# Optimization experiments

Measured on AMD Instinct MI355X. Metric: run time of the kernel, lower is better.

The kernel has to match this reference:

```python
import jax, jax.numpy as jnp
import numpy as np

DIM = 256
NUM_HEADS = 4
HEAD_DIM = DIM // NUM_HEADS
MLP_HIDDEN = int(DIM * 2.0)
SCALE = HEAD_DIM ** -0.5
LN_EPS = 1e-5


def _layernorm(x, gamma, beta):
    mu = jnp.mean(x, axis=-1, keepdims=True)
    var = jnp.mean(jnp.square(x - mu), axis=-1, keepdims=True)
    return (x - mu) * jax.lax.rsqrt(var + LN_EPS) * gamma + beta


def setup_inputs() -> dict:
    key = jax.random.key(0)
    ks = jax.random.split(key, 8)
    B, C, N, P = 8, DIM, 64, 256
    s = 0.02
    return {
        "x": jax.random.normal(ks[0], (B, C, N, P), dtype=jnp.float32),
        # torch Linear weights stored [out_features, in_features]
        "W_qkv": jax.random.normal(ks[1], (3 * DIM, DIM), dtype=jnp.float32) * s,
        "W_proj": jax.random.normal(ks[2], (DIM, DIM), dtype=jnp.float32) * s,
        "b_proj": jnp.zeros((DIM,), dtype=jnp.float32),
        "ln1_g": jnp.ones((DIM,), dtype=jnp.float32),
        "ln1_b": jnp.zeros((DIM,), dtype=jnp.float32),
        "ln2_g": jnp.ones((DIM,), dtype=jnp.float32),
        "ln2_b": jnp.zeros((DIM,), dtype=jnp.float32),
        "W_mlp1": jax.random.normal(ks[3], (MLP_HIDDEN, DIM), dtype=jnp.float32) * s,
        "b_mlp1": jnp.zeros((MLP_HIDDEN,), dtype=jnp.float32),
        "W_mlp2": jax.random.normal(ks[4], (DIM, MLP_HIDDEN), dtype=jnp.float32) * s,
        "b_mlp2": jnp.zeros((DIM,), dtype=jnp.float32),
    }


def reference(x, W_qkv, W_proj, b_proj, ln1_g, ln1_b, ln2_g, ln2_b,
              W_mlp1, b_mlp1, W_mlp2, b_mlp2):
    B, C, N, P = x.shape
    H, D = NUM_HEADS, HEAD_DIM
    # [B,C,N,P] -> [B*N, P, C]
    x_seq = jnp.transpose(x, (0, 2, 3, 1)).reshape(B * N, P, C)
    shortcut = x_seq

    h = _layernorm(x_seq, ln1_g, ln1_b)
    qkv = jnp.einsum('spc,oc->spo', h, W_qkv)              # [BN, P, 3C]
    qkv = qkv.reshape(B * N, P, 3, H, D)
    q = jnp.transpose(qkv[:, :, 0], (0, 2, 1, 3))          # [BN, H, P, D]
    k = jnp.transpose(qkv[:, :, 1], (0, 2, 1, 3))
    v = jnp.transpose(qkv[:, :, 2], (0, 2, 1, 3))

    attn = jnp.einsum('shpd,shqd->shpq', q, k) * SCALE     # [BN, H, P, P]
    attn = jax.nn.softmax(attn, axis=-1)
    o = jnp.einsum('shpq,shqd->shpd', attn, v)             # [BN, H, P, D]
    o = jnp.transpose(o, (0, 2, 1, 3)).reshape(B * N, P, C)
    o = jnp.einsum('spc,oc->spo', o, W_proj) + b_proj

    x_seq = shortcut + o

    h2 = _layernorm(x_seq, ln2_g, ln2_b)
    m = jnp.einsum('spc,oc->spo', h2, W_mlp1) + b_mlp1
    m = jax.nn.gelu(m, approximate=False)
    m = jnp.einsum('sph,oh->spo', m, W_mlp2) + b_mlp2
    x_seq = x_seq + m

    out = x_seq.reshape(B, N, P, C)
    return jnp.transpose(out, (0, 3, 1, 2))                # [B, C, N, P]
```

## Files before the change

### kernel.cpp

```cpp
#include <hip/hip_runtime.h>
#include <stdint.h>
#include <math.h>


#define DEV static __device__ __forceinline__

typedef __bf16 bf16x8 __attribute__((ext_vector_type(8)));
typedef float  f32x4  __attribute__((ext_vector_type(4)));

union B8 { bf16x8 v; uint4 q; uint32_t u[4]; uint16_t h[8]; };

DEV uint16_t f2bf(float f) {
  uint32_t u = __float_as_uint(f);
  return (uint16_t)((u + 0x7FFFu + ((u >> 16) & 1u)) >> 16);
}
DEV float bf2f(uint16_t h) { return __uint_as_float(((uint32_t)h) << 16); }
DEV uint32_t pk2(float a, float b) { return (uint32_t)f2bf(a) | ((uint32_t)f2bf(b) << 16); }

DEV f32x4 mfma16(const B8& a, const B8& b, f32x4 c) {
  return __builtin_amdgcn_mfma_f32_16x16x32_bf16(a.v, b.v, c, 0, 0, 0);
}

DEV uint32_t shfl_u(uint32_t v, int src) { return (uint32_t)__shfl((int)v, src, 64); }

DEV B8 mk(const uint32_t* w) {
  B8 x; x.u[0] = w[0]; x.u[1] = w[1]; x.u[2] = w[2]; x.u[3] = w[3]; return x;
}

DEV void xpose(const uint32_t* pk0, const uint32_t* pk1, int kd, int g, int r, uint32_t* out) {
  const int sA = 32 * (g & 1) + r;
  const int sB = sA + 16;
  const int tA = 2 * kd, tB = 2 * kd + 1;
  uint32_t a0 = shfl_u(pk0[tA], sA), b0 = shfl_u(pk0[tB], sA);
  uint32_t a1 = shfl_u(pk1[tA], sA), b1 = shfl_u(pk1[tB], sA);
  uint32_t a2 = shfl_u(pk0[tA], sB), b2 = shfl_u(pk0[tB], sB);
  uint32_t a3 = shfl_u(pk1[tA], sB), b3 = shfl_u(pk1[tB], sB);
  const bool hi = g >= 2;
  out[0] = hi ? b0 : a0;
  out[1] = hi ? b1 : a1;
  out[2] = hi ? b2 : a2;
  out[3] = hi ? b3 : a3;
}

__global__ void transformer_prep(const float* __restrict__ wqkv,
                                 const float* __restrict__ wproj,
                                 const float* __restrict__ w1,
                                 const float* __restrict__ w2,
                                 uint16_t* __restrict__ dst) {
  int e = blockIdx.x * 256 + threadIdx.x;
  const float* src; int C, local;
  if (e < 196608)      { src = wqkv;  C = 256; local = e; }
  else if (e < 262144) { src = wproj; C = 256; local = e - 196608; }
  else if (e < 393216) { src = w1;    C = 256; local = e - 262144; }
  else                 { src = w2;    C = 512; local = e - 393216; }
  int k32 = C >> 5;
  int tile = local >> 9, within = local & 511;
  int ln = within >> 3, j = within & 7;
  int tr = tile / k32, tk = tile - tr * k32;
  int row = tr * 16 + (ln & 15), col = tk * 32 + (ln >> 4) * 8 + j;
  float v = src[row * C + col];
  if (e < 65536) v *= 0.18033688011112042f;
  dst[e] = f2bf(v);
}

__global__ __launch_bounds__(1024, 4) void transformer_k1(
    const float* __restrict__ x,
    const float* __restrict__ bproj,
    const float* __restrict__ ln1g, const float* __restrict__ ln1b,
    const uint16_t* __restrict__ wf,
    uint16_t* __restrict__ osc,
    float* __restrict__ out) {
  __shared__ __attribute__((aligned(16))) uint8_t lds[65536];
  const int tid = threadIdx.x;
  const int lane = tid & 63;
  const int w = tid >> 6;
  const int r = lane & 15;
  const int g = lane >> 4;
  const int s = blockIdx.x;
  const int bb = s >> 6, nn = s & 63;
  const float* xs = x + (size_t)bb * 4194304 + (size_t)nn * 256;
  float* outp = out + (size_t)bb * 4194304 + (size_t)nn * 256;
  const f32x4 fz = {0.f, 0.f, 0.f, 0.f};

  uint32_t hfrag[8][4];
  {
    float s1 = 0.f, s2 = 0.f;
    const int p = 16 * w + r;
#pragma unroll
    for (int kt = 0; kt < 8; ++kt) {
      int c0 = 32 * kt + 8 * g;
      float v[8];
#pragma unroll
      for (int j = 0; j < 8; ++j) {
        v[j] = xs[(size_t)(c0 + j) * 16384 + p];
        s1 += v[j];
        s2 += v[j] * v[j];
      }
#pragma unroll
      for (int q = 0; q < 4; ++q) hfrag[kt][q] = pk2(v[2 * q], v[2 * q + 1]);
    }
    s1 += __shfl_xor(s1, 16, 64); s1 += __shfl_xor(s1, 32, 64);
    s2 += __shfl_xor(s2, 16, 64); s2 += __shfl_xor(s2, 32, 64);
    float mu = s1 * (1.0f / 256.0f);
    float var = s2 * (1.0f / 256.0f) - mu * mu;
    float rs = rsqrtf(var + 1e-5f);
#pragma unroll
    for (int kt = 0; kt < 8; ++kt) {
      int c0 = 32 * kt + 8 * g;
      f32x4 gA = *(const f32x4*)(ln1g + c0), gB = *(const f32x4*)(ln1g + c0 + 4);
      f32x4 bA = *(const f32x4*)(ln1b + c0), bB = *(const f32x4*)(ln1b + c0 + 4);
#pragma unroll
      for (int q = 0; q < 4; ++q) {
        uint32_t pw = hfrag[kt][q];
        float lo = bf2f((uint16_t)(pw & 0xFFFFu));
        float hi = bf2f((uint16_t)(pw >> 16));
        float glo = (q < 2) ? gA[2 * q] : gB[2 * q - 4];
        float ghi = (q < 2) ? gA[2 * q + 1] : gB[2 * q - 3];
        float blo = (q < 2) ? bA[2 * q] : bB[2 * q - 4];
        float bhi = (q < 2) ? bA[2 * q + 1] : bB[2 * q - 3];
        lo = (lo - mu) * rs * glo + blo;
        hi = (hi - mu) * rs * ghi + bhi;
        hfrag[kt][q] = pk2(lo, hi);
      }
    }
  }

#pragma unroll 1
  for (int hd = 0; hd < 4; ++hd) {
#pragma unroll
    for (int m = 0; m < 2; ++m) {
      f32x4 acc[4];
#pragma unroll
      for (int ct = 0; ct < 4; ++ct) acc[ct] = fz;
#pragma unroll
      for (int kt = 0; kt < 8; ++kt) {
        B8 a = mk(hfrag[kt]);
#pragma unroll
        for (int ct = 0; ct < 4; ++ct) {
          B8 wfr;
          wfr.q = *(const uint4*)(wf + (size_t)((((m + 1) * 16 + hd * 4 + ct) * 8 + kt) * 512) + lane * 8);
          acc[ct] = mfma16(a, wfr, acc[ct]);
        }
      }
#pragma unroll
      for (int ct = 0; ct < 4; ++ct) {
        int d = 16 * ct + r;
        int q0 = 16 * w + 4 * g;
        if (m == 0) {
#pragma unroll
          for (int i = 0; i < 4; ++i) {
            int qq = q0 + i;
            *(uint16_t*)(lds + ((qq * 128 + d * 2) ^ ((qq & 7) << 4))) = f2bf(acc[ct][i]);
          }
        } else {
          uint2 pv;
          pv.x = pk2(acc[ct][0], acc[ct][1]);
          pv.y = pk2(acc[ct][2], acc[ct][3]);
          *(uint2*)(lds + ((32768 + d * 512 + q0 * 2) ^ ((d & 7) << 4))) = pv;
        }
      }
    }
    __syncthreads();

    {
      f32x4 qT[4];
#pragma unroll
      for (int mt = 0; mt < 4; ++mt) qT[mt] = fz;
#pragma unroll
      for (int kt = 0; kt < 8; ++kt) {
        B8 hb = mk(hfrag[kt]);
#pragma unroll
        for (int mt = 0; mt < 4; ++mt) {
          B8 wa;
          wa.q = *(const uint4*)(wf + (size_t)(((hd * 4 + mt) * 8 + kt) * 512) + lane * 8);
          qT[mt] = mfma16(wa, hb, qT[mt]);
        }
      }
      uint32_t pq0[4], pq1[4];
#pragma unroll
      for (int mt = 0; mt < 4; ++mt) {
        pq0[mt] = pk2(qT[mt][0], qT[mt][1]);
        pq1[mt] = pk2(qT[mt][2], qT[mt][3]);
      }
      uint32_t qb[2][4];
#pragma unroll
      for (int kd = 0; kd < 2; ++kd) xpose(pq0, pq1, kd, g, r, qb[kd]);

      float m_ = -1e30f, l_ = 0.f;
      f32x4 oT[4];
#pragma unroll
      for (int dt = 0; dt < 4; ++dt) oT[dt] = fz;

#pragma unroll 1
      for (int chk = 0; chk < 4; ++chk) {
        f32x4 sT[4];
#pragma unroll
        for (int qt = 0; qt < 4; ++qt) sT[qt] = fz;
#pragma unroll
        for (int kd = 0; kd < 2; ++kd) {
          B8 qf = mk(qb[kd]);
#pragma unroll
          for (int qt = 0; qt < 4; ++qt) {
            int qq = chk * 64 + 16 * qt + r;
            B8 ka;
            ka.q = *(const uint4*)(lds + ((qq * 128 + (32 * kd + 8 * g) * 2) ^ ((qq & 7) << 4)));
            sT[qt] = mfma16(ka, qf, sT[qt]);
          }
        }
        float tmax = sT[0][0];
#pragma unroll
        for (int qt = 0; qt < 4; ++qt)
#pragma unroll
          for (int i = 0; i < 4; ++i) tmax = fmaxf(tmax, sT[qt][i]);
        tmax = fmaxf(tmax, __shfl_xor(tmax, 16, 64));
        tmax = fmaxf(tmax, __shfl_xor(tmax, 32, 64));
        float mn = fmaxf(m_, tmax);
        float fcor = exp2f(m_ - mn);
        float ts = 0.f;
#pragma unroll
        for (int qt = 0; qt < 4; ++qt)
#pragma unroll
          for (int i = 0; i < 4; ++i) {
            float e = exp2f(sT[qt][i] - mn);
            sT[qt][i] = e;
            ts += e;
          }
        ts += __shfl_xor(ts, 16, 64);
        ts += __shfl_xor(ts, 32, 64);
        l_ = l_ * fcor + ts;
        m_ = mn;
#pragma unroll
        for (int dt = 0; dt < 4; ++dt)
#pragma unroll
          for (int i = 0; i < 4; ++i) oT[dt][i] *= fcor;
        uint32_t pp0[4], pp1[4];
#pragma unroll
        for (int qt = 0; qt < 4; ++qt) {
          pp0[qt] = pk2(sT[qt][0], sT[qt][1]);
          pp1[qt] = pk2(sT[qt][2], sT[qt][3]);
        }
#pragma unroll
        for (int qk = 0; qk < 2; ++qk) {
          uint32_t pb[4];
          xpose(pp0, pp1, qk, g, r, pb);
          B8 pf = mk(pb);
#pragma unroll
          for (int dt = 0; dt < 4; ++dt) {
            B8 va;
            va.q = *(const uint4*)(lds + ((32768 + (16 * dt + r) * 512 + (chk * 64 + 32 * qk + 8 * g) * 2) ^ ((r & 7) << 4)));
            oT[dt] = mfma16(va, pf, oT[dt]);
          }
        }
      }
      float inv = 1.0f / l_;
      uint32_t po0[4], po1[4];
#pragma unroll
      for (int dt = 0; dt < 4; ++dt) {
        po0[dt] = pk2(oT[dt][0] * inv, oT[dt][1] * inv);
        po1[dt] = pk2(oT[dt][2] * inv, oT[dt][3] * inv);
      }
#pragma unroll
      for (int kd = 0; kd < 2; ++kd) {
        uint32_t ofr[4];
        xpose(po0, po1, kd, g, r, ofr);
        B8 t; t.u[0] = ofr[0]; t.u[1] = ofr[1]; t.u[2] = ofr[2]; t.u[3] = ofr[3];
        *(uint4*)(osc + (size_t)((s * 16 + w) * 8 + 2 * hd + kd) * 512 + lane * 8) = t.q;
      }
    }
    __syncthreads();
  }

#pragma unroll 1
  for (int q3 = 0; q3 < 4; ++q3) {
    f32x4 acc[4];
#pragma unroll
    for (int ct = 0; ct < 4; ++ct) acc[ct] = fz;
#pragma unroll
    for (int kt = 0; kt < 8; ++kt) {
      B8 a;
      a.q = *(const uint4*)(osc + (size_t)((s * 16 + w) * 8 + kt) * 512 + lane * 8);
#pragma unroll
      for (int ct = 0; ct < 4; ++ct) {
        B8 wfr;
        wfr.q = *(const uint4*)(wf + 196608 + (size_t)(((q3 * 4 + ct) * 8 + kt) * 512) + lane * 8);
        acc[ct] = mfma16(a, wfr, acc[ct]);
      }
    }
#pragma unroll
    for (int ct = 0; ct < 4; ++ct) {
      int c = q3 * 64 + 16 * ct + r;
      float bias = bproj[c];
      int p0 = 16 * w + 4 * g;
      f32x4 res = *(const f32x4*)(xs + (size_t)c * 16384 + p0);
      f32x4 x2v;
#pragma unroll
      for (int i = 0; i < 4; ++i) x2v[i] = acc[ct][i] + bias + res[i];
      *(f32x4*)(outp + (size_t)c * 16384 + p0) = x2v;
    }
  }
}

__global__ __launch_bounds__(1024, 4) void transformer_k2(
    const float* __restrict__ ln2g, const float* __restrict__ ln2b,
    const uint16_t* __restrict__ w1f, const uint16_t* __restrict__ w2f,
    const float* __restrict__ bm1, const float* __restrict__ bm2,
    float* __restrict__ out) {
  __shared__ __attribute__((aligned(16))) uint8_t lds[106496];
  const int tid = threadIdx.x;
  const int lane = tid & 63;
  const int w = tid >> 6;
  const int r = lane & 15, g = lane >> 4;
  const int bid = blockIdx.x;
  const int s = bid >> 2, tg = bid & 3;
  const int bb = s >> 6, nn = s & 63;
  float* outp = out + (size_t)bb * 4194304 + (size_t)nn * 256;
  const int tokbase = tg * 64;
  const f32x4 fz = {0.f, 0.f, 0.f, 0.f};

  float v[16];
  {
    float s1 = 0.f, s2 = 0.f;
    const int p = tokbase + lane;
#pragma unroll
    for (int j = 0; j < 16; ++j) {
      float t = outp[(size_t)(w * 16 + j) * 16384 + p];
      v[j] = t;
      s1 += t;
      s2 += t * t;
    }
    float2 pr; pr.x = s1; pr.y = s2;
    *(float2*)(lds + 98304 + (w * 64 + lane) * 8) = pr;
  }
  __syncthreads();
  {
    float su = 0.f, sq = 0.f;
#pragma unroll
    for (int w2 = 0; w2 < 16; ++w2) {
      float2 pr = *(const float2*)(lds + 98304 + (w2 * 64 + lane) * 8);
      su += pr.x;
      sq += pr.y;
    }
    float mu = su * (1.0f / 256.0f);
    float var = sq * (1.0f / 256.0f) - mu * mu;
    float rs = rsqrtf(var + 1e-5f);
    uint32_t pk[8];
#pragma unroll
    for (int q = 0; q < 4; ++q) {
      int c0 = w * 16 + q * 4;
      f32x4 gv = *(const f32x4*)(ln2g + c0);
      f32x4 bv = *(const f32x4*)(ln2b + c0);
      float n0 = (v[q * 4 + 0] - mu) * rs * gv[0] + bv[0];
      float n1 = (v[q * 4 + 1] - mu) * rs * gv[1] + bv[1];
      float n2 = (v[q * 4 + 2] - mu) * rs * gv[2] + bv[2];
      float n3 = (v[q * 4 + 3] - mu) * rs * gv[3] + bv[3];
      pk[q * 2 + 0] = pk2(n0, n1);
      pk[q * 2 + 1] = pk2(n2, n3);
    }
    const int mt = lane >> 4;
    const int kt = w >> 1;
#pragma unroll
    for (int hblk = 0; hblk < 2; ++hblk) {
      int lanep = (lane & 15) + 32 * (w & 1) + 16 * hblk;
      uint4 t;
      t.x = pk[hblk * 4 + 0]; t.y = pk[hblk * 4 + 1];
      t.z = pk[hblk * 4 + 2]; t.w = pk[hblk * 4 + 3];
      *(uint4*)(lds + (mt * 8 + kt) * 1024 + lanep * 16) = t;
    }
  }
  __syncthreads();

  f32x4 acc1[4][2];
#pragma unroll
  for (int mt = 0; mt < 4; ++mt)
#pragma unroll
    for (int nt = 0; nt < 2; ++nt) acc1[mt][nt] = fz;
#pragma unroll
  for (int kt = 0; kt < 8; ++kt) {
    B8 a[4];
#pragma unroll
    for (int mt = 0; mt < 4; ++mt)
      a[mt].q = *(const uint4*)(lds + (mt * 8 + kt) * 1024 + lane * 16);
#pragma unroll
    for (int nt = 0; nt < 2; ++nt) {
      B8 bfr;
      bfr.q = *(const uint4*)(w1f + (size_t)(((2 * w + nt) * 8 + kt) * 512) + lane * 8);
#pragma unroll
      for (int mt = 0; mt < 4; ++mt) acc1[mt][nt] = mfma16(a[mt], bfr, acc1[mt][nt]);
    }
  }
#pragma unroll
  for (int nt = 0; nt < 2; ++nt) {
    float bias = bm1[(2 * w + nt) * 16 + r];
#pragma unroll
    for (int mt = 0; mt < 4; ++mt) {
#pragma unroll
      for (int i = 0; i < 4; ++i) {
        float vv = acc1[mt][nt][i] + bias;
        vv = 0.5f * vv * (1.0f + erff(vv * 0.70710678118654752440f));
        int lanep = (4 * g + i) + 16 * (2 * nt + (r >> 3));
        *(uint16_t*)(lds + 32768 + (mt * 16 + w) * 1024 + lanep * 16 + (r & 7) * 2) = f2bf(vv);
      }
    }
  }
  __syncthreads();

  f32x4 acc2[4];
#pragma unroll
  for (int mt = 0; mt < 4; ++mt) acc2[mt] = fz;
#pragma unroll
  for (int kt = 0; kt < 16; ++kt) {
    B8 bfr;
    bfr.q = *(const uint4*)(w2f + (size_t)((w * 16 + kt) * 512) + lane * 8);
#pragma unroll
    for (int mt = 0; mt < 4; ++mt) {
      B8 a;
      a.q = *(const uint4*)(lds + 32768 + (mt * 16 + kt) * 1024 + lane * 16);
      acc2[mt] = mfma16(a, bfr, acc2[mt]);
    }
  }

  {
    int c = w * 16 + r;
    float bias = bm2[c];
#pragma unroll
    for (int mt = 0; mt < 4; ++mt) {
      int p0 = tokbase + 16 * mt + 4 * g;
      f32x4 res = *(const f32x4*)(outp + (size_t)c * 16384 + p0);
      f32x4 o;
#pragma unroll
      for (int i = 0; i < 4; ++i) o[i] = res[i] + acc2[mt][i] + bias;
      *(f32x4*)(outp + (size_t)c * 16384 + p0) = o;
    }
  }
}

extern "C" void kernel_launch(void* const* d_in, const int* in_sizes, int n_in,
                              void* d_out, int out_size, void* d_ws, size_t ws_size,
                              hipStream_t stream) {
  (void)in_sizes; (void)n_in; (void)out_size; (void)ws_size;
  const float* x     = (const float*)d_in[0];
  const float* wqkv  = (const float*)d_in[1];
  const float* wproj = (const float*)d_in[2];
  const float* bproj = (const float*)d_in[3];
  const float* ln1g  = (const float*)d_in[4];
  const float* ln1b  = (const float*)d_in[5];
  const float* ln2g  = (const float*)d_in[6];
  const float* ln2b  = (const float*)d_in[7];
  const float* w1    = (const float*)d_in[8];
  const float* bm1   = (const float*)d_in[9];
  const float* w2    = (const float*)d_in[10];
  const float* bm2   = (const float*)d_in[11];
  uint16_t* wbf = (uint16_t*)d_ws;
  uint16_t* osc = wbf + 524288;
  float* out = (float*)d_out;

  transformer_prep<<<2048, 256, 0, stream>>>(wqkv, wproj, w1, w2, wbf);
  transformer_k1<<<512, 1024, 0, stream>>>(x, bproj, ln1g, ln1b, wbf, osc, out);
  transformer_k2<<<2048, 1024, 0, stream>>>(ln2g, ln2b, wbf + 262144, wbf + 393216, bm1, bm2, out);
}
```

Baseline: 710.5 us.

## Split fused transformer block into five staged kernels with global intermediates

Replaces the two large fused kernels (attention block per sequence with 1024 threads, MLP block) with five 256-thread kernels: LN1+QKV projection writing Q/K/V fragments to workspace, per-head attention, output projection plus residual with LN2 statistics, MLP1 with GELU, and MLP2 plus residual. The intent is finer-grained parallelism, higher occupancy and larger per-wave MFMA tiles, in place of one block serially looping over heads. The cost is large bf16 intermediate traffic through global memory (Q, K, V, MLP hidden activations) and extra kernel launches.

```diff
diff --git a/kernel.cpp b/kernel.cpp
--- a/kernel.cpp
+++ b/kernel.cpp
@@ -20,11 +20,18 @@
 DEV f32x4 mfma16(const B8& a, const B8& b, f32x4 c) {
   return __builtin_amdgcn_mfma_f32_16x16x32_bf16(a.v, b.v, c, 0, 0, 0);
 }
-
 DEV uint32_t shfl_u(uint32_t v, int src) { return (uint32_t)__shfl((int)v, src, 64); }
-
-DEV B8 mk(const uint32_t* w) {
-  B8 x; x.u[0] = w[0]; x.u[1] = w[1]; x.u[2] = w[2]; x.u[3] = w[3]; return x;
+DEV f32x4 vmax4(f32x4 a, f32x4 b) {
+  f32x4 o;
+  o[0] = fmaxf(a[0], b[0]); o[1] = fmaxf(a[1], b[1]);
+  o[2] = fmaxf(a[2], b[2]); o[3] = fmaxf(a[3], b[3]);
+  return o;
+}
+DEV f32x4 shfl4x(f32x4 v, int m) {
+  f32x4 o;
+#pragma unroll
+  for (int i = 0; i < 4; ++i) o[i] = __shfl_xor(v[i], m, 64);
+  return o;
 }
 
 DEV void xpose(const uint32_t* pk0, const uint32_t* pk1, int kd, int g, int r, uint32_t* out) {
@@ -63,373 +70,517 @@
   dst[e] = f2bf(v);
 }
 
-__global__ __launch_bounds__(1024, 4) void transformer_k1(
+__global__ __launch_bounds__(256, 2) void transformer_kA(
     const float* __restrict__ x,
-    const float* __restrict__ bproj,
     const float* __restrict__ ln1g, const float* __restrict__ ln1b,
-    const uint16_t* __restrict__ wf,
-    uint16_t* __restrict__ osc,
-    float* __restrict__ out) {
-  __shared__ __attribute__((aligned(16))) uint8_t lds[65536];
+    const uint16_t* __restrict__ wqkvf,
+    uint16_t* __restrict__ qf, uint16_t* __restrict__ kf,
+    uint16_t* __restrict__ vt) {
+  __shared__ __attribute__((aligned(16))) uint8_t lds[76800];
   const int tid = threadIdx.x;
   const int lane = tid & 63;
-  const int w = tid >> 6;
-  const int r = lane & 15;
-  const int g = lane >> 4;
-  const int s = blockIdx.x;
-  const int bb = s >> 6, nn = s & 63;
-  const float* xs = x + (size_t)bb * 4194304 + (size_t)nn * 256;
-  float* outp = out + (size_t)bb * 4194304 + (size_t)nn * 256;
-  const f32x4 fz = {0.f, 0.f, 0.f, 0.f};
-
-  uint32_t hfrag[8][4];
-  {
-    float s1 = 0.f, s2 = 0.f;
-    const int p = 16 * w + r;
-#pragma unroll
-    for (int kt = 0; kt < 8; ++kt) {
-      int c0 = 32 * kt + 8 * g;
-      float v[8];
-#pragma unroll
-      for (int j = 0; j < 8; ++j) {
-        v[j] = xs[(size_t)(c0 + j) * 16384 + p];
-        s1 += v[j];
-        s2 += v[j] * v[j];
-      }
-#pragma unroll
-      for (int q = 0; q < 4; ++q) hfrag[kt][q] = pk2(v[2 * q], v[2 * q + 1]);
-    }
-    s1 += __shfl_xor(s1, 16, 64); s1 += __shfl_xor(s1, 32, 64);
-    s2 += __shfl_xor(s2, 16, 64); s2 += __shfl_xor(s2, 32, 64);
-    float mu = s1 * (1.0f / 256.0f);
-    float var = s2 * (1.0f / 256.0f) - mu * mu;
-    float rs = rsqrtf(var + 1e-5f);
-#pragma unroll
-    for (int kt = 0; kt < 8; ++kt) {
-      int c0 = 32 * kt + 8 * g;
-      f32x4 gA = *(const f32x4*)(ln1g + c0), gB = *(const f32x4*)(ln1g + c0 + 4);
-      f32x4 bA = *(const f32x4*)(ln1b + c0), bB = *(const f32x4*)(ln1b + c0 + 4);
-#pragma unroll
-      for (int q = 0; q < 4; ++q) {
-        uint32_t pw = hfrag[kt][q];
-        float lo = bf2f((uint16_t)(pw & 0xFFFFu));
-        float hi = bf2f((uint16_t)(pw >> 16));
-        float glo = (q < 2) ? gA[2 * q] : gB[2 * q - 4];
-        float ghi = (q < 2) ? gA[2 * q + 1] : gB[2 * q - 3];
-        float blo = (q < 2) ? bA[2 * q] : bB[2 * q - 4];
-        float bhi = (q < 2) ? bA[2 * q + 1] : bB[2 * q - 3];
-        lo = (lo - mu) * rs * glo + blo;
-        hi = (hi - mu) * rs * ghi + bhi;
-        hfrag[kt][q] = pk2(lo, hi);
-      }
-    }
-  }
-
-#pragma unroll 1
-  for (int hd = 0; hd < 4; ++hd) {
-#pragma unroll
-    for (int m = 0; m < 2; ++m) {
-      f32x4 acc[4];
-#pragma unroll
-      for (int ct = 0; ct < 4; ++ct) acc[ct] = fz;
-#pragma unroll
-      for (int kt = 0; kt < 8; ++kt) {
-        B8 a = mk(hfrag[kt]);
-#pragma unroll
-        for (int ct = 0; ct < 4; ++ct) {
-          B8 wfr;
-          wfr.q = *(const uint4*)(wf + (size_t)((((m + 1) * 16 + hd * 4 + ct) * 8 + kt) * 512) + lane * 8);
-          acc[ct] = mfma16(a, wfr, acc[ct]);
-        }
-      }
-#pragma unroll
-      for (int ct = 0; ct < 4; ++ct) {
-        int d = 16 * ct + r;
-        int q0 = 16 * w + 4 * g;
-        if (m == 0) {
-#pragma unroll
-          for (int i = 0; i < 4; ++i) {
-            int qq = q0 + i;
-            *(uint16_t*)(lds + ((qq * 128 + d * 2) ^ ((qq & 7) << 4))) = f2bf(acc[ct][i]);
-          }
-        } else {
-          uint2 pv;
-          pv.x = pk2(acc[ct][0], acc[ct][1]);
-          pv.y = pk2(acc[ct][2], acc[ct][3]);
-          *(uint2*)(lds + ((32768 + d * 512 + q0 * 2) ^ ((d & 7) << 4))) = pv;
-        }
-      }
-    }
-    __syncthreads();
-
-    {
-      f32x4 qT[4];
-#pragma unroll
-      for (int mt = 0; mt < 4; ++mt) qT[mt] = fz;
-#pragma unroll
-      for (int kt = 0; kt < 8; ++kt) {
-        B8 hb = mk(hfrag[kt]);
-#pragma unroll
-        for (int mt = 0; mt < 4; ++mt) {
-          B8 wa;
-          wa.q = *(const uint4*)(wf + (size_t)(((hd * 4 + mt) * 8 + kt) * 512) + lane * 8);
-          qT[mt] = mfma16(wa, hb, qT[mt]);
-        }
-      }
-      uint32_t pq0[4], pq1[4];
-#pragma unroll
-      for (int mt = 0; mt < 4; ++mt) {
-        pq0[mt] = pk2(qT[mt][0], qT[mt][1]);
-        pq1[mt] = pk2(qT[mt][2], qT[mt][3]);
-      }
-      uint32_t qb[2][4];
-#pragma unroll
-      for (int kd = 0; kd < 2; ++kd) xpose(pq0, pq1, kd, g, r, qb[kd]);
-
-      float m_ = -1e30f, l_ = 0.f;
-      f32x4 oT[4];
-#pragma unroll
-      for (int dt = 0; dt < 4; ++dt) oT[dt] = fz;
-
-#pragma unroll 1
-      for (int chk = 0; chk < 4; ++chk) {
-        f32x4 sT[4];
-#pragma unroll
-        for (int qt = 0; qt < 4; ++qt) sT[qt] = fz;
-#pragma unroll
-        for (int kd = 0; kd < 2; ++kd) {
-          B8 qf = mk(qb[kd]);
-#pragma unroll
-          for (int qt = 0; qt < 4; ++qt) {
-            int qq = chk * 64 + 16 * qt + r;
-            B8 ka;
-            ka.q = *(const uint4*)(lds + ((qq * 128 + (32 * kd + 8 * g) * 2) ^ ((qq & 7) << 4)));
-            sT[qt] = mfma16(ka, qf, sT[qt]);
-          }
-        }
-        float tmax = sT[0][0];
-#pragma unroll
-        for (int qt = 0; qt < 4; ++qt)
-#pragma unroll
-          for (int i = 0; i < 4; ++i) tmax = fmaxf(tmax, sT[qt][i]);
-        tmax = fmaxf(tmax, __shfl_xor(tmax, 16, 64));
-        tmax = fmaxf(tmax, __shfl_xor(tmax, 32, 64));
-        float mn = fmaxf(m_, tmax);
-        float fcor = exp2f(m_ - mn);
-        float ts = 0.f;
-#pragma unroll
-        for (int qt = 0; qt < 4; ++qt)
-#pragma unroll
-          for (int i = 0; i < 4; ++i) {
-            float e = exp2f(sT[qt][i] - mn);
-            sT[qt][i] = e;
-            ts += e;
-          }
-        ts += __shfl_xor(ts, 16, 64);
-        ts += __shfl_xor(ts, 32, 64);
-        l_ = l_ * fcor + ts;
-        m_ = mn;
-#pragma unroll
-        for (int dt = 0; dt < 4; ++dt)
-#pragma unroll
-          for (int i = 0; i < 4; ++i) oT[dt][i] *= fcor;
-        uint32_t pp0[4], pp1[4];
-#pragma unroll
-        for (int qt = 0; qt < 4; ++qt) {
-          pp0[qt] = pk2(sT[qt][0], sT[qt][1]);
-          pp1[qt] = pk2(sT[qt][2], sT[qt][3]);
-        }
-#pragma unroll
-        for (int qk = 0; qk < 2; ++qk) {
-          uint32_t pb[4];
-          xpose(pp0, pp1, qk, g, r, pb);
-          B8 pf = mk(pb);
-#pragma unroll
-          for (int dt = 0; dt < 4; ++dt) {
-            B8 va;
-            va.q = *(const uint4*)(lds + ((32768 + (16 * dt + r) * 512 + (chk * 64 + 32 * qk + 8 * g) * 2) ^ ((r & 7) << 4)));
-            oT[dt] = mfma16(va, pf, oT[dt]);
-          }
-        }
-      }
-      float inv = 1.0f / l_;
-      uint32_t po0[4], po1[4];
-#pragma unroll
-      for (int dt = 0; dt < 4; ++dt) {
-        po0[dt] = pk2(oT[dt][0] * inv, oT[dt][1] * inv);
-        po1[dt] = pk2(oT[dt][2] * inv, oT[dt][3] * inv);
-      }
-#pragma unroll
-      for (int kd = 0; kd < 2; ++kd) {
-        uint32_t ofr[4];
-        xpose(po0, po1, kd, g, r, ofr);
-        B8 t; t.u[0] = ofr[0]; t.u[1] = ofr[1]; t.u[2] = ofr[2]; t.u[3] = ofr[3];
-        *(uint4*)(osc + (size_t)((s * 16 + w) * 8 + 2 * hd + kd) * 512 + lane * 8) = t.q;
-      }
-    }
-    __syncthreads();
-  }
-
-#pragma unroll 1
-  for (int q3 = 0; q3 < 4; ++q3) {
-    f32x4 acc[4];
-#pragma unroll
-    for (int ct = 0; ct < 4; ++ct) acc[ct] = fz;
-#pragma unroll
-    for (int kt = 0; kt < 8; ++kt) {
-      B8 a;
-      a.q = *(const uint4*)(osc + (size_t)((s * 16 + w) * 8 + kt) * 512 + lane * 8);
-#pragma unroll
-      for (int ct = 0; ct < 4; ++ct) {
-        B8 wfr;
-        wfr.q = *(const uint4*)(wf + 196608 + (size_t)(((q3 * 4 + ct) * 8 + kt) * 512) + lane * 8);
-        acc[ct] = mfma16(a, wfr, acc[ct]);
-      }
-    }
-#pragma unroll
-    for (int ct = 0; ct < 4; ++ct) {
-      int c = q3 * 64 + 16 * ct + r;
-      float bias = bproj[c];
-      int p0 = 16 * w + 4 * g;
-      f32x4 res = *(const f32x4*)(xs + (size_t)c * 16384 + p0);
-      f32x4 x2v;
-#pragma unroll
-      for (int i = 0; i < 4; ++i) x2v[i] = acc[ct][i] + bias + res[i];
-      *(f32x4*)(outp + (size_t)c * 16384 + p0) = x2v;
-    }
-  }
-}
-
-__global__ __launch_bounds__(1024, 4) void transformer_k2(
-    const float* __restrict__ ln2g, const float* __restrict__ ln2b,
-    const uint16_t* __restrict__ w1f, const uint16_t* __restrict__ w2f,
-    const float* __restrict__ bm1, const float* __restrict__ bm2,
-    float* __restrict__ out) {
-  __shared__ __attribute__((aligned(16))) uint8_t lds[106496];
-  const int tid = threadIdx.x;
-  const int lane = tid & 63;
-  const int w = tid >> 6;
+  const int wv = tid >> 6;
   const int r = lane & 15, g = lane >> 4;
   const int bid = blockIdx.x;
-  const int s = bid >> 2, tg = bid & 3;
-  const int bb = s >> 6, nn = s & 63;
-  float* outp = out + (size_t)bb * 4194304 + (size_t)nn * 256;
-  const int tokbase = tg * 64;
+  const int s = bid >> 2, q64 = bid & 3;
+  const int tok0 = q64 * 64;
+  const float* xs = x + (size_t)(s >> 6) * 4194304 + (size_t)(s & 63) * 256 + tok0;
   const f32x4 fz = {0.f, 0.f, 0.f, 0.f};
 
-  float v[16];
+  ((float*)(lds + 74752))[tid] = ln1g[tid];
+  ((float*)(lds + 75776))[tid] = ln1b[tid];
+
   {
-    float s1 = 0.f, s2 = 0.f;
-    const int p = tokbase + lane;
+    const int pg = tid & 15, cq = tid >> 4;
+    const int p4 = pg * 4;
+    f32x4 s1 = fz, s2 = fz;
 #pragma unroll
     for (int j = 0; j < 16; ++j) {
-      float t = outp[(size_t)(w * 16 + j) * 16384 + p];
-      v[j] = t;
-      s1 += t;
-      s2 += t * t;
-    }
-    float2 pr; pr.x = s1; pr.y = s2;
-    *(float2*)(lds + 98304 + (w * 64 + lane) * 8) = pr;
+      int c = j * 16 + cq;
+      f32x4 v = *(const f32x4*)(xs + (size_t)c * 16384 + p4);
+      s1 += v; s2 += v * v;
+      uint2 w; w.x = pk2(v[0], v[1]); w.y = pk2(v[2], v[3]);
+      *(uint2*)(lds + c * 132 + p4 * 2) = w;
+    }
+    *(f32x4*)(lds + 66560 + (cq * 16 + pg) * 32) = s1;
+    *(f32x4*)(lds + 66560 + (cq * 16 + pg) * 32 + 16) = s2;
   }
   __syncthreads();
+
   {
+    const int tokl = 16 * wv + r;
+    const int pg = tokl >> 2, e = tokl & 3;
     float su = 0.f, sq = 0.f;
 #pragma unroll
-    for (int w2 = 0; w2 < 16; ++w2) {
-      float2 pr = *(const float2*)(lds + 98304 + (w2 * 64 + lane) * 8);
-      su += pr.x;
-      sq += pr.y;
+    for (int cq = 0; cq < 16; ++cq) {
+      su += *(const float*)(lds + 66560 + (cq * 16 + pg) * 32 + e * 4);
+      sq += *(const float*)(lds + 66560 + (cq * 16 + pg) * 32 + 16 + e * 4);
     }
     float mu = su * (1.0f / 256.0f);
     float var = sq * (1.0f / 256.0f) - mu * mu;
     float rs = rsqrtf(var + 1e-5f);
-    uint32_t pk[8];
-#pragma unroll
-    for (int q = 0; q < 4; ++q) {
-      int c0 = w * 16 + q * 4;
-      f32x4 gv = *(const f32x4*)(ln2g + c0);
-      f32x4 bv = *(const f32x4*)(ln2b + c0);
-      float n0 = (v[q * 4 + 0] - mu) * rs * gv[0] + bv[0];
-      float n1 = (v[q * 4 + 1] - mu) * rs * gv[1] + bv[1];
-      float n2 = (v[q * 4 + 2] - mu) * rs * gv[2] + bv[2];
-      float n3 = (v[q * 4 + 3] - mu) * rs * gv[3] + bv[3];
-      pk[q * 2 + 0] = pk2(n0, n1);
-      pk[q * 2 + 1] = pk2(n2, n3);
-    }
-    const int mt = lane >> 4;
-    const int kt = w >> 1;
-#pragma unroll
-    for (int hblk = 0; hblk < 2; ++hblk) {
-      int lanep = (lane & 15) + 32 * (w & 1) + 16 * hblk;
-      uint4 t;
-      t.x = pk[hblk * 4 + 0]; t.y = pk[hblk * 4 + 1];
-      t.z = pk[hblk * 4 + 2]; t.w = pk[hblk * 4 + 3];
-      *(uint4*)(lds + (mt * 8 + kt) * 1024 + lanep * 16) = t;
+#pragma unroll
+    for (int tk = 0; tk < 8; ++tk) {
+      int c0 = 32 * tk + 8 * g;
+      uint32_t pk[4];
+#pragma unroll
+      for (int q = 0; q < 4; ++q) {
+        float lo, hi;
+        {
+          int c = c0 + 2 * q;
+          uint16_t raw = *(const uint16_t*)(lds + c * 132 + tokl * 2);
+          float gg = ((const float*)(lds + 74752))[c];
+          float bb = ((const float*)(lds + 75776))[c];
+          lo = (bf2f(raw) - mu) * rs * gg + bb;
+        }
+        {
+          int c = c0 + 2 * q + 1;
+          uint16_t raw = *(const uint16_t*)(lds + c * 132 + tokl * 2);
+          float gg = ((const float*)(lds + 74752))[c];
+          float bb = ((const float*)(lds + 75776))[c];
+          hi = (bf2f(raw) - mu) * rs * gg + bb;
+        }
+        pk[q] = pk2(lo, hi);
+      }
+      uint4 t; t.x = pk[0]; t.y = pk[1]; t.z = pk[2]; t.w = pk[3];
+      *(uint4*)(lds + 33792 + (wv * 8 + tk) * 1024 + lane * 16) = t;
     }
   }
   __syncthreads();
 
-  f32x4 acc1[4][2];
-#pragma unroll
-  for (int mt = 0; mt < 4; ++mt)
-#pragma unroll
-    for (int nt = 0; nt < 2; ++nt) acc1[mt][nt] = fz;
+#pragma unroll 1
+  for (int pp = 0; pp < 3; ++pp) {
+    const int n0 = wv * 192 + pp * 64;
+    const int mi = n0 >> 8, hd = (n0 >> 6) & 3;
+    const int s4hd = s * 4 + hd;
+    f32x4 acc[4][4];
+#pragma unroll
+    for (int a = 0; a < 4; ++a)
+#pragma unroll
+      for (int b = 0; b < 4; ++b) acc[a][b] = fz;
+
+    if (mi < 2) {
+#pragma unroll
+      for (int kt = 0; kt < 8; ++kt) {
+        B8 hf[4];
+#pragma unroll
+        for (int tt = 0; tt < 4; ++tt)
+          hf[tt].q = *(const uint4*)(lds + 33792 + (tt * 8 + kt) * 1024 + lane * 16);
+#pragma unroll
+        for (int nt = 0; nt < 4; ++nt) {
+          B8 wf_;
+          wf_.q = *(const uint4*)(wqkvf + (size_t)((((n0 >> 4) + nt) * 8 + kt) * 512) + lane * 8);
+#pragma unroll
+          for (int tt = 0; tt < 4; ++tt) acc[nt][tt] = mfma16(wf_, hf[tt], acc[nt][tt]);
+        }
+      }
+      uint16_t* dstb = (mi == 0) ? qf : kf;
+#pragma unroll
+      for (int tt = 0; tt < 4; ++tt) {
+        uint32_t p0[4], p1[4];
+#pragma unroll
+        for (int nt = 0; nt < 4; ++nt) {
+          p0[nt] = pk2(acc[nt][tt][0], acc[nt][tt][1]);
+          p1[nt] = pk2(acc[nt][tt][2], acc[nt][tt][3]);
+        }
+        int qtg = q64 * 4 + tt;
+#pragma unroll
+        for (int kd = 0; kd < 2; ++kd) {
+          uint32_t ofr[4];
+          xpose(p0, p1, kd, g, r, ofr);
+          uint4 t; t.x = ofr[0]; t.y = ofr[1]; t.z = ofr[2]; t.w = ofr[3];
+          *(uint4*)(dstb + (size_t)(((s4hd * 16 + qtg) * 2 + kd) * 512) + lane * 8) = t;
+        }
+      }
+    } else {
+#pragma unroll
+      for (int kt = 0; kt < 8; ++kt) {
+        B8 hf[4];
+#pragma unroll
+        for (int rt = 0; rt < 4; ++rt)
+          hf[rt].q = *(const uint4*)(lds + 33792 + (rt * 8 + kt) * 1024 + lane * 16);
+#pragma unroll
+        for (int ct = 0; ct < 4; ++ct) {
+          B8 wf_;
+          wf_.q = *(const uint4*)(wqkvf + (size_t)((((n0 >> 4) + ct) * 8 + kt) * 512) + lane * 8);
+#pragma unroll
+          for (int rt = 0; rt < 4; ++rt) acc[rt][ct] = mfma16(hf[rt], wf_, acc[rt][ct]);
+        }
+      }
+#pragma unroll
+      for (int rt = 0; rt < 4; ++rt) {
+#pragma unroll
+        for (int ct = 0; ct < 4; ++ct) {
+          int d = 16 * ct + r;
+          int tokr = tok0 + 16 * rt + 4 * g;
+          uint2 pv;
+          pv.x = pk2(acc[rt][ct][0], acc[rt][ct][1]);
+          pv.y = pk2(acc[rt][ct][2], acc[rt][ct][3]);
+          *(uint2*)(vt + (size_t)(s4hd * 64 + d) * 256 + tokr) = pv;
+        }
+      }
+    }
+  }
+}
+
+__global__ __launch_bounds__(256, 2) void transformer_kB(
+    uint16_t* __restrict__ qf, const uint16_t* __restrict__ kf,
+    const uint16_t* __restrict__ vt) {
+  __shared__ __attribute__((aligned(16))) uint8_t lds[81920];
+  const int tid = threadIdx.x;
+  const int lane = tid & 63;
+  const int wv = tid >> 6;
+  const int r = lane & 15, g = lane >> 4;
+  const int bid = blockIdx.x;
+  const int s4hd = bid;
+  const f32x4 fz = {0.f, 0.f, 0.f, 0.f};
+
+#pragma unroll
+  for (int i = 0; i < 8; ++i) {
+    int off = i * 256 + tid;
+    *(uint4*)(lds + off * 16) = *(const uint4*)(kf + (size_t)s4hd * 16384 + off * 8);
+  }
+#pragma unroll
+  for (int i = 0; i < 8; ++i) {
+    int f = i * 256 + tid;
+    int d = f >> 5, t8 = (f & 31) * 8;
+    uint4 v = *(const uint4*)(vt + (size_t)s4hd * 16384 + d * 256 + t8);
+    *(uint4*)(lds + 32768 + ((d * 512 + t8 * 2) ^ ((d & 7) << 4))) = v;
+  }
+  __syncthreads();
+
+  uint8_t* Plds = lds + 65536 + wv * 4096;
+
+#pragma unroll 1
+  for (int qt4 = 0; qt4 < 4; ++qt4) {
+    const int qtg = wv * 4 + qt4;
+    B8 qb[2];
+#pragma unroll
+    for (int kd = 0; kd < 2; ++kd)
+      qb[kd].q = *(const uint4*)(qf + (size_t)(((s4hd * 16 + qtg) * 2 + kd) * 512) + lane * 8);
+
+    f32x4 sT[16];
+#pragma unroll
+    for (int kt = 0; kt < 16; ++kt) sT[kt] = fz;
+#pragma unroll
+    for (int kt = 0; kt < 16; ++kt) {
+#pragma unroll
+      for (int kd = 0; kd < 2; ++kd) {
+        B8 ka;
+        ka.q = *(const uint4*)(lds + (kt * 2 + kd) * 1024 + lane * 16);
+        sT[kt] = mfma16(ka, qb[kd], sT[kt]);
+      }
+    }
+    f32x4 t8v[8];
+#pragma unroll
+    for (int i = 0; i < 8; ++i) t8v[i] = vmax4(sT[i], sT[i + 8]);
+#pragma unroll
+    for (int i = 0; i < 4; ++i) t8v[i] = vmax4(t8v[i], t8v[i + 4]);
+    f32x4 tm = vmax4(vmax4(t8v[0], t8v[1]), vmax4(t8v[2], t8v[3]));
+    float mx = fmaxf(fmaxf(tm[0], tm[1]), fmaxf(tm[2], tm[3]));
+    mx = fmaxf(mx, __shfl_xor(mx, 16, 64));
+    mx = fmaxf(mx, __shfl_xor(mx, 32, 64));
+    f32x4 ss = fz;
+#pragma unroll
+    for (int kt = 0; kt < 16; ++kt) {
+#pragma unroll
+      for (int i = 0; i < 4; ++i) sT[kt][i] = exp2f(sT[kt][i] - mx);
+      ss += sT[kt];
+    }
+    float l = ss[0] + ss[1] + ss[2] + ss[3];
+    l += __shfl_xor(l, 16, 64);
+    l += __shfl_xor(l, 32, 64);
+    float inv = 1.0f / l;
+
+    f32x4 oT[4];
+#pragma unroll
+    for (int dt = 0; dt < 4; ++dt) oT[dt] = fz;
+#pragma unroll
+    for (int kh = 0; kh < 2; ++kh) {
+#pragma unroll
+      for (int kt8 = 0; kt8 < 8; ++kt8) {
+        int kt = kh * 8 + kt8;
+        uint2 pv;
+        pv.x = pk2(sT[kt][0], sT[kt][1]);
+        pv.y = pk2(sT[kt][2], sT[kt][3]);
+        *(uint2*)(Plds + ((r * 256 + kt8 * 32 + 8 * g) ^ ((r & 7) << 4))) = pv;
+      }
+#pragma unroll
+      for (int ks = 0; ks < 4; ++ks) {
+        B8 pb;
+        pb.q = *(const uint4*)(Plds + ((r * 256 + ks * 64 + 16 * g) ^ ((r & 7) << 4)));
+#pragma unroll
+        for (int dt = 0; dt < 4; ++dt) {
+          int d = 16 * dt + r;
+          B8 va;
+          va.q = *(const uint4*)(lds + 32768 + ((d * 512 + (128 * kh + 32 * ks + 8 * g) * 2) ^ ((d & 7) << 4)));
+          oT[dt] = mfma16(va, pb, oT[dt]);
+        }
+      }
+    }
+#pragma unroll
+    for (int dt = 0; dt < 4; ++dt) {
+      uint2 ov;
+      ov.x = pk2(oT[dt][0] * inv, oT[dt][1] * inv);
+      ov.y = pk2(oT[dt][2] * inv, oT[dt][3] * inv);
+      *(uint2*)(qf + (size_t)s4hd * 16384 + (16 * qtg + r) * 64 + 16 * dt + 4 * g) = ov;
+    }
+  }
+}
+
+__global__ __launch_bounds__(256, 2) void transformer_kC(
+    const float* __restrict__ x, const float* __restrict__ bproj,
+    const uint16_t* __restrict__ wprojf,
+    const uint16_t* __restrict__ o,
+    float2* __restrict__ stats,
+    float* __restrict__ out) {
+  __shared__ __attribute__((aligned(16))) uint8_t lds[34816];
+  const int tid = threadIdx.x;
+  const int lane = tid & 63;
+  const int wv = tid >> 6;
+  const int r = lane & 15, g = lane >> 4;
+  const int bid = blockIdx.x;
+  const int s = bid >> 2, q64 = bid & 3;
+  const int tok0 = q64 * 64;
+  const float* xs = x + (size_t)(s >> 6) * 4194304 + (size_t)(s & 63) * 256;
+  float* outp = out + (size_t)(s >> 6) * 4194304 + (size_t)(s & 63) * 256;
+  const f32x4 fz = {0.f, 0.f, 0.f, 0.f};
+
+#pragma unroll
+  for (int tk = 0; tk < 8; ++tk) {
+    int c0 = 32 * tk + 8 * g;
+    int hd = c0 >> 6, d0 = c0 & 63;
+    int tok = tok0 + 16 * wv + r;
+    uint4 v = *(const uint4*)(o + (size_t)(s * 4 + hd) * 16384 + tok * 64 + d0);
+    *(uint4*)(lds + (wv * 8 + tk) * 1024 + lane * 16) = v;
+  }
+  __syncthreads();
+
+  const int n0 = wv * 64;
+  f32x4 acc[4][4];
+#pragma unroll
+  for (int a = 0; a < 4; ++a)
+#pragma unroll
+    for (int b = 0; b < 4; ++b) acc[a][b] = fz;
 #pragma unroll
   for (int kt = 0; kt < 8; ++kt) {
+    B8 of[4];
+#pragma unroll
+    for (int rt = 0; rt < 4; ++rt)
+      of[rt].q = *(const uint4*)(lds + (rt * 8 + kt) * 1024 + lane * 16);
+#pragma unroll
+    for (int ct = 0; ct < 4; ++ct) {
+      B8 wf_;
+      wf_.q = *(const uint4*)(wprojf + (size_t)((((n0 >> 4) + ct) * 8 + kt) * 512) + lane * 8);
+#pragma unroll
+      for (int rt = 0; rt < 4; ++rt) acc[rt][ct] = mfma16(of[rt], wf_, acc[rt][ct]);
+    }
+  }
+  f32x4 s1a[4], s2a[4];
+#pragma unroll
+  for (int rt = 0; rt < 4; ++rt) { s1a[rt] = fz; s2a[rt] = fz; }
+#pragma unroll
+  for (int ct = 0; ct < 4; ++ct) {
+    int c = n0 + 16 * ct + r;
+    float bias = bproj[c];
+#pragma unroll
+    for (int rt = 0; rt < 4; ++rt) {
+      int p = tok0 + 16 * rt + 4 * g;
+      f32x4 res = *(const f32x4*)(xs + (size_t)c * 16384 + p);
+      f32x4 x2v;
+#pragma unroll
+      for (int i = 0; i < 4; ++i) x2v[i] = acc[rt][ct][i] + bias + res[i];
+      *(f32x4*)(outp + (size_t)c * 16384 + p) = x2v;
+      s1a[rt] += x2v;
+      s2a[rt] += x2v * x2v;
+    }
+  }
+#pragma unroll
+  for (int rt = 0; rt < 4; ++rt) {
+#pragma unroll
+    for (int m = 1; m < 16; m <<= 1) {
+      s1a[rt] += shfl4x(s1a[rt], m);
+      s2a[rt] += shfl4x(s2a[rt], m);
+    }
+  }
+  if (r == 0) {
+#pragma unroll
+    for (int rt = 0; rt < 4; ++rt)
+#pragma unroll
+      for (int i = 0; i < 4; ++i) {
+        float2 pr; pr.x = s1a[rt][i]; pr.y = s2a[rt][i];
+        *(float2*)(lds + 32768 + ((16 * rt + 4 * g + i) * 4 + wv) * 8) = pr;
+      }
+  }
+  __syncthreads();
+  if (tid < 64) {
+    float su = 0.f, sq = 0.f;
+#pragma unroll
+    for (int w2 = 0; w2 < 4; ++w2) {
+      float2 pr = *(const float2*)(lds + 32768 + (tid * 4 + w2) * 8);
+      su += pr.x; sq += pr.y;
+    }
+    float mu = su * (1.0f / 256.0f);
+    float var = sq * (1.0f / 256.0f) - mu * mu;
+    float2 st; st.x = mu; st.y = rsqrtf(var + 1e-5f);
+    stats[bid * 64 + tid] = st;
+  }
+}
+
+__global__ __launch_bounds__(256, 2) void transformer_kD(
+    const float* __restrict__ ln2g, const float* __restrict__ ln2b,
+    const uint16_t* __restrict__ w1f, const float* __restrict__ bm1,
+    const float2* __restrict__ stats,
+    const float* __restrict__ out,
+    uint16_t* __restrict__ mf) {
+  __shared__ __attribute__((aligned(16))) uint8_t lds[66560];
+  const int tid = threadIdx.x;
+  const int lane = tid & 63;
+  const int wv = tid >> 6;
+  const int r = lane & 15, g = lane >> 4;
+  const int bid = blockIdx.x;
+  const int s = bid >> 2, q64 = bid & 3;
+  const int tok0 = q64 * 64;
+  const float* outp = out + (size_t)(s >> 6) * 4194304 + (size_t)(s & 63) * 256;
+  const f32x4 fz = {0.f, 0.f, 0.f, 0.f};
+
+  {
+    const int pg = tid & 15, cq = tid >> 4;
+    const int p4 = pg * 4;
+    float2 st[4];
+#pragma unroll
+    for (int e = 0; e < 4; ++e) st[e] = stats[bid * 64 + p4 + e];
+#pragma unroll
+    for (int j = 0; j < 16; ++j) {
+      int c = j * 16 + cq;
+      f32x4 v = *(const f32x4*)(outp + (size_t)c * 16384 + tok0 + p4);
+      float gg = ln2g[c];
+      float bb = ln2b[c];
+      float n0v = (v[0] - st[0].x) * st[0].y * gg + bb;
+      float n1v = (v[1] - st[1].x) * st[1].y * gg + bb;
+      float n2v = (v[2] - st[2].x) * st[2].y * gg + bb;
+      float n3v = (v[3] - st[3].x) * st[3].y * gg + bb;
+      uint2 w; w.x = pk2(n0v, n1v); w.y = pk2(n2v, n3v);
+      *(uint2*)(lds + c * 132 + p4 * 2) = w;
+    }
+  }
+  __syncthreads();
+  {
+    const int tokl = 16 * wv + r;
+#pragma unroll
+    for (int tk = 0; tk < 8; ++tk) {
+      int c0 = 32 * tk + 8 * g;
+      uint32_t pk[4];
+#pragma unroll
+      for (int q = 0; q < 4; ++q) {
+        uint16_t a = *(const uint16_t*)(lds + (c0 + 2 * q) * 132 + tokl * 2);
+        uint16_t b = *(const uint16_t*)(lds + (c0 + 2 * q + 1) * 132 + tokl * 2);
+        pk[q] = (uint32_t)a | ((uint32_t)b << 16);
+      }
+      uint4 t; t.x = pk[0]; t.y = pk[1]; t.z = pk[2]; t.w = pk[3];
+      *(uint4*)(lds + 33792 + (wv * 8 + tk) * 1024 + lane * 16) = t;
+    }
+  }
+  __syncthreads();
+
+#pragma unroll 1
+  for (int pp = 0; pp < 2; ++pp) {
+    const int n0 = wv * 128 + pp * 64;
+    f32x4 acc[4][4];
+#pragma unroll
+    for (int a = 0; a < 4; ++a)
+#pragma unroll
+      for (int b = 0; b < 4; ++b) acc[a][b] = fz;
+#pragma unroll
+    for (int kt = 0; kt < 8; ++kt) {
+      B8 hf[4];
+#pragma unroll
+      for (int tt = 0; tt < 4; ++tt)
+        hf[tt].q = *(const uint4*)(lds + 33792 + (tt * 8 + kt) * 1024 + lane * 16);
+#pragma unroll
+      for (int nt = 0; nt < 4; ++nt) {
+        B8 wf_;
+        wf_.q = *(const uint4*)(w1f + (size_t)((((n0 >> 4) + nt) * 8 + kt) * 512) + lane * 8);
+#pragma unroll
+        for (int tt = 0; tt < 4; ++tt) acc[nt][tt] = mfma16(wf_, hf[tt], acc[nt][tt]);
+      }
+    }
+#pragma unroll
+    for (int nt = 0; nt < 4; ++nt) {
+      f32x4 b4 = *(const f32x4*)(bm1 + n0 + 16 * nt + 4 * g);
+#pragma unroll
+      for (int tt = 0; tt < 4; ++tt) {
+#pragma unroll
+        for (int i = 0; i < 4; ++i) {
+          float vv = acc[nt][tt][i] + b4[i];
+          acc[nt][tt][i] = 0.5f * vv * (1.0f + erff(vv * 0.70710678118654752440f));
+        }
+      }
+    }
+#pragma unroll
+    for (int tt = 0; tt < 4; ++tt) {
+      uint32_t p0[4], p1[4];
+#pragma unroll
+      for (int nt = 0; nt < 4; ++nt) {
+        p0[nt] = pk2(acc[nt][tt][0], acc[nt][tt][1]);
+        p1[nt] = pk2(acc[nt][tt][2], acc[nt][tt][3]);
+      }
+#pragma unroll
+      for (int kd = 0; kd < 2; ++kd) {
+        uint32_t ofr[4];
+        xpose(p0, p1, kd, g, r, ofr);
+        uint4 t; t.x = ofr[0]; t.y = ofr[1]; t.z = ofr[2]; t.w = ofr[3];
+        *(uint4*)(mf + (size_t)(((bid * 4 + tt) * 16 + (n0 >> 5) + kd) * 512) + lane * 8) = t;
+      }
+    }
+  }
+}
+
+__global__ __launch_bounds__(256, 2) void transformer_kE(
+    const uint16_t* __restrict__ w2f, const float* __restrict__ bm2,
+    const uint16_t* __restrict__ mf,
+    float* __restrict__ out) {
+  const int tid = threadIdx.x;
+  const int lane = tid & 63;
+  const int wv = tid >> 6;
+  const int r = lane & 15, g = lane >> 4;
+  const int bid = blockIdx.x;
+  const int s = bid >> 2, q64 = bid & 3;
+  const int tok0 = q64 * 64;
+  float* outp = out + (size_t)(s >> 6) * 4194304 + (size_t)(s & 63) * 256;
+  const f32x4 fz = {0.f, 0.f, 0.f, 0.f};
+
+  f32x4 acc[4][4];
+#pragma unroll
+  for (int a = 0; a < 4; ++a)
+#pragma unroll
+    for (int b = 0; b < 4; ++b) acc[a][b] = fz;
+#pragma unroll
+  for (int kt = 0; kt < 16; ++kt) {
     B8 a[4];
 #pragma unroll
-    for (int mt = 0; mt < 4; ++mt)
-      a[mt].q = *(const uint4*)(lds + (mt * 8 + kt) * 1024 + lane * 16);
-#pragma unroll
-    for (int nt = 0; nt < 2; ++nt) {
-      B8 bfr;
-      bfr.q = *(const uint4*)(w1f + (size_t)(((2 * w + nt) * 8 + kt) * 512) + lane * 8);
-#pragma unroll
-      for (int mt = 0; mt < 4; ++mt) acc1[mt][nt] = mfma16(a[mt], bfr, acc1[mt][nt]);
-    }
-  }
-#pragma unroll
-  for (int nt = 0; nt < 2; ++nt) {
-    float bias = bm1[(2 * w + nt) * 16 + r];
-#pragma unroll
-    for (int mt = 0; mt < 4; ++mt) {
-#pragma unroll
-      for (int i = 0; i < 4; ++i) {
-        float vv = acc1[mt][nt][i] + bias;
-        vv = 0.5f * vv * (1.0f + erff(vv * 0.70710678118654752440f));
-        int lanep = (4 * g + i) + 16 * (2 * nt + (r >> 3));
-        *(uint16_t*)(lds + 32768 + (mt * 16 + w) * 1024 + lanep * 16 + (r & 7) * 2) = f2bf(vv);
-      }
-    }
-  }
-  __syncthreads();
-
-  f32x4 acc2[4];
-#pragma unroll
-  for (int mt = 0; mt < 4; ++mt) acc2[mt] = fz;
-#pragma unroll
-  for (int kt = 0; kt < 16; ++kt) {
-    B8 bfr;
-    bfr.q = *(const uint4*)(w2f + (size_t)((w * 16 + kt) * 512) + lane * 8);
-#pragma unroll
-    for (int mt = 0; mt < 4; ++mt) {
-      B8 a;
-      a.q = *(const uint4*)(lds + 32768 + (mt * 16 + kt) * 1024 + lane * 16);
-      acc2[mt] = mfma16(a, bfr, acc2[mt]);
-    }
-  }
-
-  {
-    int c = w * 16 + r;
+    for (int rt = 0; rt < 4; ++rt)
+      a[rt].q = *(const uint4*)(mf + (size_t)(((bid * 4 + rt) * 16 + kt) * 512) + lane * 8);
+#pragma unroll
+    for (int ct = 0; ct < 4; ++ct) {
+      B8 wf_;
+      wf_.q = *(const uint4*)(w2f + (size_t)(((wv * 4 + ct) * 16 + kt) * 512) + lane * 8);
+#pragma unroll
+      for (int rt = 0; rt < 4; ++rt) acc[rt][ct] = mfma16(a[rt], wf_, acc[rt][ct]);
+    }
+  }
+#pragma unroll
+  for (int ct = 0; ct < 4; ++ct) {
+    int c = wv * 64 + 16 * ct + r;
     float bias = bm2[c];
 #pragma unroll
-    for (int mt = 0; mt < 4; ++mt) {
-      int p0 = tokbase + 16 * mt + 4 * g;
-      f32x4 res = *(const f32x4*)(outp + (size_t)c * 16384 + p0);
+    for (int rt = 0; rt < 4; ++rt) {
+      int p = tok0 + 16 * rt + 4 * g;
+      f32x4 res = *(const f32x4*)(outp + (size_t)c * 16384 + p);
       f32x4 o;
 #pragma unroll
-      for (int i = 0; i < 4; ++i) o[i] = res[i] + acc2[mt][i] + bias;
-      *(f32x4*)(outp + (size_t)c * 16384 + p0) = o;
+      for (int i = 0; i < 4; ++i) o[i] = res[i] + acc[rt][ct][i] + bias;
+      *(f32x4*)(outp + (size_t)c * 16384 + p) = o;
     }
   }
 }
@@ -450,11 +601,20 @@
   const float* bm1   = (const float*)d_in[9];
   const float* w2    = (const float*)d_in[10];
   const float* bm2   = (const float*)d_in[11];
-  uint16_t* wbf = (uint16_t*)d_ws;
-  uint16_t* osc = wbf + 524288;
   float* out = (float*)d_out;
 
+  uint16_t* ws16 = (uint16_t*)d_ws;
+  uint16_t* wbf  = ws16;
+  float2*  stats = (float2*)((char*)d_ws + 1048576);
+  uint16_t* qfrag = ws16 + 1048576;
+  uint16_t* kfrag = qfrag + 33554432;
+  uint16_t* vtb   = kfrag + 33554432;
+  uint16_t* mfrag = qfrag;
+
   transformer_prep<<<2048, 256, 0, stream>>>(wqkv, wproj, w1, w2, wbf);
-  transformer_k1<<<512, 1024, 0, stream>>>(x, bproj, ln1g, ln1b, wbf, osc, out);
-  transformer_k2<<<2048, 1024, 0, stream>>>(ln2g, ln2b, wbf + 262144, wbf + 393216, bm1, bm2, out);
-}
+  transformer_kA<<<2048, 256, 0, stream>>>(x, ln1g, ln1b, wbf, qfrag, kfrag, vtb);
+  transformer_kB<<<2048, 256, 0, stream>>>(qfrag, kfrag, vtb);
+  transformer_kC<<<2048, 256, 0, stream>>>(x, bproj, wbf + 196608, qfrag, stats, out);
+  transformer_kD<<<2048, 256, 0, stream>>>(ln2g, ln2b, wbf + 262144, bm1, stats, out, mfrag);
+  transformer_kE<<<2048, 256, 0, stream>>>(wbf + 393216, bm2, mfrag, out);
+}
```

Measured after the change: 1.017 ms. +43.1%, slower.
